# Performance work log

Measured on AMD Instinct MI355X. Metric: run time of the kernel, lower is better.

The kernel has to match this reference:

```python
import jax, jax.numpy as jnp
import numpy as np

VOXEL_SIZE = 0.1
MAX_GS_PER_VOXEL = 2
CONF_W, OPAC_W = 0.7, 0.3
CONF_THRESH, OPAC_THRESH = 0.1, 0.01
VOX_OFFSET, VOX_BITS = 512, 10  # pack 3 voxel coords into 30-bit int32 key


def _erp_directions(H, W, img_h, img_w):
    # Equirectangular ray directions, [H, W, 3]
    fx = img_w / (2.0 * np.pi)
    fy = -img_h / np.pi
    cx, cy = img_w / 2.0, img_h / 2.0
    u = jnp.arange(W, dtype=jnp.float32)
    v = jnp.arange(H, dtype=jnp.float32)
    uu, vv = jnp.meshgrid(u, v, indexing='xy')  # [H, W]
    lon = (uu + 0.5 - cx) / fx
    lat = (vv + 0.5 - cy) / fy
    cos_lat = jnp.cos(lat)
    return jnp.stack([cos_lat * jnp.sin(lon), jnp.sin(-lat), cos_lat * jnp.cos(lon)], axis=-1)


def _select_per_batch(vid, neg_score, valid_i):
    # vid: [P] int32 voxel ids (invalid -> INT32_MAX sentinel, sorts last)
    # per-voxel top-k by score via sort + segmented rank; returns bool [P] selection mask
    P = vid.shape[0]
    idx = jnp.arange(P, dtype=jnp.int32)
    vid_s, _, idx_s, valid_s = jax.lax.sort((vid, neg_score, idx, valid_i), num_keys=2)
    is_new = jnp.concatenate([jnp.ones((1,), bool), vid_s[1:] != vid_s[:-1]])
    seg_start = jax.lax.cummax(jnp.where(is_new, idx, 0), axis=0)
    rank = idx - seg_start  # rank within voxel, best score first
    sel_s = (rank < MAX_GS_PER_VOXEL) & (valid_s == 1)
    return jnp.zeros((P,), bool).at[idx_s].set(sel_s)


def _forward(depth, covariance, rotation, opacity, sh_color, confidence, poses, img_h, img_w):
    B, N, H, W = depth.shape
    P = N * H * W
    dirs = _erp_directions(H, W, img_h, img_w)  # [H,W,3]
    pts_cam = depth[..., None] * dirs  # [B,N,H,W,3]
    R = poses[:, :, :3, :3]
    t = poses[:, :, :3, 3]
    pts_world = jnp.einsum('bnij,bnhwj->bnhwi', R, pts_cam) + t[:, :, None, None, :]
    means = pts_world.reshape(B, P, 3)
    scales = covariance.transpose(0, 1, 3, 4, 2).reshape(B, P, 3)
    rots = rotation.transpose(0, 1, 3, 4, 2).reshape(B, P, 4)
    opac = opacity.reshape(B, P, 1)
    shs = sh_color.transpose(0, 1, 3, 4, 2).reshape(B, P, -1)
    conf = confidence.reshape(B, P, 1)
    valid = (conf[..., 0] > CONF_THRESH) & (opac[..., 0] > OPAC_THRESH)
    score = CONF_W * conf[..., 0] + OPAC_W * opac[..., 0]
    # voxel binning: packed 30-bit voxel id per point
    vc = jnp.clip(jnp.floor(means / VOXEL_SIZE).astype(jnp.int32) + VOX_OFFSET, 0, (1 << VOX_BITS) - 1)
    vid = (vc[..., 0] << (2 * VOX_BITS)) | (vc[..., 1] << VOX_BITS) | vc[..., 2]
    vid = jnp.where(valid, vid, jnp.int32(2**31 - 1))
    sel = jax.vmap(_select_per_batch)(vid, -score, valid.astype(jnp.int32))  # [B,P]
    feat = jnp.concatenate([means, scales, rots, opac, shs, conf], axis=-1)  # [B,P,24]
    return feat * sel[..., None].astype(feat.dtype), sel


def setup_inputs() -> dict:
    key = jax.random.key(0)
    ks = jax.random.split(key, 7)
    B, N, H, W, C = 2, 4, 256, 512, 12
    return {
        'depth': jax.random.uniform(ks[0], (B, N, H, W), jnp.float32),
        'covariance': jax.random.uniform(ks[1], (B, N, 3, H, W), jnp.float32),
        'rotation': jax.random.normal(ks[2], (B, N, 4, H, W), jnp.float32),
        'opacity': jax.random.uniform(ks[3], (B, N, H, W), jnp.float32),
        'sh_color': jax.random.normal(ks[4], (B, N, C, H, W), jnp.float32),
        'confidence': jax.random.uniform(ks[5], (B, N, H, W), jnp.float32),
        'poses': jax.random.normal(ks[6], (B, N, 4, 4), jnp.float32),
        'img_h': 256,
        'img_w': 512,
    }


def reference(depth, covariance, rotation, opacity, sh_color, confidence, poses, img_h, img_w):
    return _forward(depth, covariance, rotation, opacity, sh_color, confidence, poses, img_h, img_w)
```

## Files before the change

### kernel.cpp

```cpp
#include <hip/hip_runtime.h>
#include <stdint.h>
#include <math.h>

#ifndef M_PI
#define M_PI 3.14159265358979323846
#endif

#define B_ 2
#define N_ 4
#define H_ 256
#define W_ 512
#define C_ 12
#define HW_ (H_*W_)
#define P_ (N_*HW_)
#define BP_ (B_*P_)
#define INVALID_ENTRY 0xFFFFFFFFu

#define CHUNK 1024
#define PPT 4
#define LTAB 2048
#define LMASK (LTAB-1)
#define PROBE_MAX 8

__device__ __forceinline__ uint32_t mix32(uint32_t k) {
    k ^= k >> 16; k *= 0x85ebca6bu;
    k ^= k >> 13; k *= 0xc2b2ae35u;
    k ^= k >> 16;
    return k;
}

__device__ __forceinline__ void compute_means(
    int b, int n, float d, const float* __restrict__ tab,
    const float* __restrict__ poses, int h, int w, float m[3])
{
    float sin_lon  = tab[w];
    float cos_lon  = tab[W_ + w];
    float cos_lat  = tab[2*W_ + h];
    float sin_nlat = tab[2*W_ + H_ + h];

    float pc0 = __fmul_rn(d, __fmul_rn(cos_lat, sin_lon));
    float pc1 = __fmul_rn(d, sin_nlat);
    float pc2 = __fmul_rn(d, __fmul_rn(cos_lat, cos_lon));

    const float* Pz = poses + (size_t)(b * N_ + n) * 16;
#pragma unroll
    for (int i = 0; i < 3; ++i) {
        float s = __fmul_rn(Pz[i*4+0], pc0);
        s = __fadd_rn(s, __fmul_rn(Pz[i*4+1], pc1));
        s = __fadd_rn(s, __fmul_rn(Pz[i*4+2], pc2));
        s = __fadd_rn(s, Pz[i*4+3]);
        m[i] = s;
    }
}

__device__ __forceinline__ unsigned long long make_pk(float conf, float opac, int p) {
    float score = __fadd_rn(__fmul_rn(0.7f, conf), __fmul_rn(0.3f, opac));
    return ((unsigned long long)__float_as_uint(score) << 32)
         | (unsigned long long)(~(uint32_t)p);
}

__device__ __forceinline__ uint32_t voxel_key(const float m[3], int b) {
    int vc[3];
#pragma unroll
    for (int i = 0; i < 3; ++i) {
        float q  = __fdiv_rn(m[i], 0.1f);
        float fq = floorf(q);
        int vi = (int)fq + 512;
        vi = vi < 0 ? 0 : (vi > 1023 ? 1023 : vi);
        vc[i] = vi;
    }
    uint32_t vid = ((uint32_t)vc[0] << 20) | ((uint32_t)vc[1] << 10) | (uint32_t)vc[2];
    return vid | ((uint32_t)b << 30) | 0x80000000u;
}

__device__ __forceinline__ uint32_t gfind(uint32_t* __restrict__ keys,
                                          uint32_t key, uint32_t tmask) {
    uint32_t slot = mix32(key) & tmask;
    while (true) {
        uint32_t k = keys[slot];
        if (k == key) return slot;
        if (k == 0u) {
            uint32_t prev = atomicCAS(&keys[slot], 0u, key);
            if (prev == 0u || prev == key) return slot;
        }
        slot = (slot + 1) & tmask;
    }
}

__device__ __forceinline__ void gmerge(ulonglong2* __restrict__ slots, uint32_t slot,
                                       unsigned long long a, unsigned long long b) {
    ulonglong2 sp = slots[slot];
    unsigned long long low = a;
    if (a > sp.x) {
        unsigned long long old = atomicMax(&slots[slot].x, a);
        low = old < a ? old : a;
    }
    unsigned long long push = low > b ? low : b;
    if (push != 0ull && push > sp.y) atomicMax(&slots[slot].y, push);
}

__global__ __launch_bounds__(256) void k_dirs(
    const int* __restrict__ p_imh, const int* __restrict__ p_imw,
    float* __restrict__ tab)
{
    int i = blockIdx.x * blockDim.x + threadIdx.x;
    int imh = *p_imh, imw = *p_imw;
    float fxf = (float)((double)imw / (2.0 * M_PI));
    float fyf = (float)(-(double)imh / M_PI);
    float cxf = (float)imw * 0.5f;
    float cyf = (float)imh * 0.5f;
    if (i < W_) {
        float lon = __fdiv_rn(__fsub_rn(__fadd_rn((float)i, 0.5f), cxf), fxf);
        double dlon = (double)lon;
        tab[i]       = (float)sin(dlon);
        tab[W_ + i]  = (float)cos(dlon);
    } else if (i < W_ + H_) {
        int h = i - W_;
        float lat = __fdiv_rn(__fsub_rn(__fadd_rn((float)h, 0.5f), cyf), fyf);
        double dlat = (double)lat;
        tab[2*W_ + h]       = (float)cos(dlat);
        tab[2*W_ + H_ + h]  = (float)sin(-dlat);
    }
}

__global__ __launch_bounds__(256) void k_pass1(
    const float* __restrict__ depth,
    const float* __restrict__ opacity,
    const float* __restrict__ confidence,
    const float* __restrict__ poses,
    const float* __restrict__ tab,
    uint32_t* __restrict__ keys,
    ulonglong2* __restrict__ slots,
    uint32_t* __restrict__ entry_arr,
    uint32_t tmask)
{
    __shared__ uint32_t           lkey[LTAB];
    __shared__ unsigned long long ls0[LTAB];
    __shared__ unsigned long long ls1[LTAB];
    __shared__ uint32_t           lgs[LTAB];

    for (int i = threadIdx.x; i < LTAB; i += 256) {
        lkey[i] = 0u; ls0[i] = 0ull; ls1[i] = 0ull;
    }
    __syncthreads();

    const int base = blockIdx.x * CHUNK;

    uint32_t           mykey[PPT];
    unsigned long long mypk[PPT];
    int                myl[PPT];

#pragma unroll
    for (int k = 0; k < PPT; ++k) {
        int g  = base + threadIdx.x + k * 256;
        int b  = g >> 19;
        int p  = g & (P_ - 1);
        int n  = p >> 17;
        int hw = p & (HW_ - 1);
        int h  = hw >> 9;
        int w  = hw & (W_ - 1);

        float conf = confidence[g];
        float opac = opacity[g];
        bool valid = (conf > 0.1f) && (opac > 0.01f);
        myl[k] = -1;
        if (!valid) continue;

        float m[3];
        compute_means(b, n, depth[g], tab, poses, h, w, m);
        uint32_t key = voxel_key(m, b);
        unsigned long long pk = make_pk(conf, opac, p);
        mykey[k] = key; mypk[k] = pk;

        uint32_t sl = mix32(key) & LMASK;
        int found = -1;
#pragma unroll 1
        for (int pr = 0; pr < PROBE_MAX; ++pr) {
            uint32_t kk = atomicCAS(&lkey[sl], 0u, key);
            if (kk == 0u || kk == key) { found = (int)sl; break; }
            sl = (sl + 1) & LMASK;
        }
        if (found >= 0) {
            unsigned long long old = atomicMax(&ls0[found], pk);
            unsigned long long low = old < pk ? old : pk;
            if (low != 0ull) atomicMax(&ls1[found], low);
            myl[k] = found;
        } else {
            myl[k] = -2;
        }
    }
    __syncthreads();

    for (int i = threadIdx.x; i < LTAB; i += 256) {
        uint32_t key = lkey[i];
        if (key == 0u) continue;
        uint32_t slot = gfind(keys, key, tmask);
        lgs[i] = slot;
        gmerge(slots, slot, ls0[i], ls1[i]);
    }
    __syncthreads();

#pragma unroll
    for (int k = 0; k < PPT; ++k) {
        int g = base + threadIdx.x + k * 256;
        uint32_t e;
        if (myl[k] == -1) {
            e = INVALID_ENTRY;
        } else if (myl[k] >= 0) {
            e = lgs[myl[k]];
        } else {
            uint32_t slot = gfind(keys, mykey[k], tmask);
            gmerge(slots, slot, mypk[k], 0ull);
            e = slot;
        }
        entry_arr[g] = e;
    }
}

__global__ __launch_bounds__(256) void k_pass3(
    const float* __restrict__ depth,
    const float* __restrict__ covariance,
    const float* __restrict__ rotation,
    const float* __restrict__ opacity,
    const float* __restrict__ sh_color,
    const float* __restrict__ confidence,
    const float* __restrict__ poses,
    const float* __restrict__ tab,
    const uint32_t* __restrict__ entry_arr,
    const ulonglong2* __restrict__ slots,
    float* __restrict__ out)
{
    int g = blockIdx.x * blockDim.x + threadIdx.x;
    if (g >= BP_) return;
    int b  = g >> 19;
    int p  = g & (P_ - 1);
    int n  = p >> 17;
    int hw = p & (HW_ - 1);
    int h  = hw >> 9;
    int w  = hw & (W_ - 1);

    float conf = confidence[g];
    float opac = opacity[g];

    uint32_t e = entry_arr[g];
    bool sel = false;
    if (e != INVALID_ENTRY) {
        unsigned long long pk = make_pk(conf, opac, p);
        ulonglong2 sp = slots[e];
        sel = (pk == sp.x) || (pk == sp.y);
    }

    alignas(16) float v[24];
    if (sel) {
        float m[3];
        compute_means(b, n, depth[g], tab, poses, h, w, m);
        int bn = b * N_ + n;
        const float* cov = covariance + (size_t)bn * 3  * HW_ + hw;
        const float* rot = rotation   + (size_t)bn * 4  * HW_ + hw;
        const float* shc = sh_color   + (size_t)bn * 12 * HW_ + hw;
        v[0] = m[0]; v[1] = m[1]; v[2] = m[2];
        v[3] = cov[0]; v[4] = cov[HW_]; v[5] = cov[2*HW_];
        v[6] = rot[0]; v[7] = rot[HW_]; v[8] = rot[2*HW_]; v[9] = rot[3*HW_];
        v[10] = opac;
#pragma unroll
        for (int c = 0; c < 12; ++c) v[11 + c] = shc[(size_t)c * HW_];
        v[23] = conf;
    } else {
#pragma unroll
        for (int i = 0; i < 24; ++i) v[i] = 0.0f;
    }

    float4* o = (float4*)(out + (size_t)g * 24);
#pragma unroll
    for (int i = 0; i < 6; ++i) o[i] = ((const float4*)v)[i];

    out[(size_t)BP_ * 24 + g] = sel ? 1.0f : 0.0f;
}

extern "C" void kernel_launch(void* const* d_in, const int* in_sizes, int n_in,
                              void* d_out, int out_size, void* d_ws, size_t ws_size,
                              hipStream_t stream)
{
    const float* depth      = (const float*)d_in[0];
    const float* covariance = (const float*)d_in[1];
    const float* rotation   = (const float*)d_in[2];
    const float* opacity    = (const float*)d_in[3];
    const float* sh_color   = (const float*)d_in[4];
    const float* confidence = (const float*)d_in[5];
    const float* poses      = (const float*)d_in[6];
    const int*   imh        = (const int*)d_in[7];
    const int*   imw        = (const int*)d_in[8];
    float* out = (float*)d_out;

    size_t tab_bytes = (size_t)(2*W_ + 2*H_) * 4;
    size_t fixed_bytes = (size_t)BP_ * 4 + tab_bytes;
    size_t T = (size_t)1 << 20;
    while (T > ((size_t)1 << 18) && fixed_bytes + T * 20 > ws_size) T >>= 1;

    char* wp = (char*)d_ws;
    uint32_t* keys     = (uint32_t*)wp;   wp += T * 4;
    ulonglong2* slots  = (ulonglong2*)wp; wp += T * 16;
    uint32_t* entry_a  = (uint32_t*)wp;   wp += (size_t)BP_ * 4;
    float* tab = (float*)wp;              wp += tab_bytes;

    hipMemsetAsync(d_ws, 0x00, T * 20, stream);

    dim3 blk(256);
    hipLaunchKernelGGL(k_dirs, dim3((2*W_ + 2*H_ + 255) / 256), blk, 0, stream,
                       imh, imw, tab);

    hipLaunchKernelGGL(k_pass1, dim3(BP_ / CHUNK), blk, 0, stream,
                       depth, opacity, confidence, poses, tab,
                       keys, slots, entry_a, (uint32_t)(T - 1));
    hipLaunchKernelGGL(k_pass3, dim3(BP_ / 256), blk, 0, stream,
                       depth, covariance, rotation, opacity, sh_color, confidence,
                       poses, tab, entry_a, slots, out);
}
```

Baseline: 307.3 us.

## Stage pass3 outputs through LDS for coalesced nontemporal vector stores

Pass3 now loads every feature for all points without branching, multiplies each by the selection mask, and writes them into a transposed shared-memory tile. It then writes coalesced float4 rows to the output with nontemporal stores. Previously each thread wrote six strided float4s and loaded features only for selected points. This improves write coalescing and keeps streaming output out of cache, but reads all inputs even for unselected points and adds LDS traffic plus a barrier. Pass1 also reuses the lkey array for global slot ids, dropping the separate lgs array to cut shared memory.

```diff
diff --git a/kernel.cpp b/kernel.cpp
--- a/kernel.cpp
+++ b/kernel.cpp
@@ -22,6 +22,8 @@
 #define LMASK (LTAB-1)
 #define PROBE_MAX 8
 
+typedef float fx4 __attribute__((ext_vector_type(4)));
+
 __device__ __forceinline__ uint32_t mix32(uint32_t k) {
     k ^= k >> 16; k *= 0x85ebca6bu;
     k ^= k >> 13; k *= 0xc2b2ae35u;
@@ -29,15 +31,10 @@
     return k;
 }
 
-__device__ __forceinline__ void compute_means(
-    int b, int n, float d, const float* __restrict__ tab,
-    const float* __restrict__ poses, int h, int w, float m[3])
-{
-    float sin_lon  = tab[w];
-    float cos_lon  = tab[W_ + w];
-    float cos_lat  = tab[2*W_ + h];
-    float sin_nlat = tab[2*W_ + H_ + h];
-
+__device__ __forceinline__ void compute_means_raw(
+    int b, int n, float d, float sin_lon, float cos_lon, float cos_lat, float sin_nlat,
+    const float* __restrict__ poses, float m[3])
+{
     float pc0 = __fmul_rn(d, __fmul_rn(cos_lat, sin_lon));
     float pc1 = __fmul_rn(d, sin_nlat);
     float pc2 = __fmul_rn(d, __fmul_rn(cos_lat, cos_lon));
@@ -51,6 +48,14 @@
         s = __fadd_rn(s, Pz[i*4+3]);
         m[i] = s;
     }
+}
+
+__device__ __forceinline__ void compute_means(
+    int b, int n, float d, const float* __restrict__ tab,
+    const float* __restrict__ poses, int h, int w, float m[3])
+{
+    compute_means_raw(b, n, d, tab[w], tab[W_ + w], tab[2*W_ + h], tab[2*W_ + H_ + h],
+                      poses, m);
 }
 
 __device__ __forceinline__ unsigned long long make_pk(float conf, float opac, int p) {
@@ -137,7 +142,6 @@
     __shared__ uint32_t           lkey[LTAB];
     __shared__ unsigned long long ls0[LTAB];
     __shared__ unsigned long long ls1[LTAB];
-    __shared__ uint32_t           lgs[LTAB];
 
     for (int i = threadIdx.x; i < LTAB; i += 256) {
         lkey[i] = 0u; ls0[i] = 0ull; ls1[i] = 0ull;
@@ -195,8 +199,8 @@
         uint32_t key = lkey[i];
         if (key == 0u) continue;
         uint32_t slot = gfind(keys, key, tmask);
-        lgs[i] = slot;
         gmerge(slots, slot, ls0[i], ls1[i]);
+        lkey[i] = slot;
     }
     __syncthreads();
 
@@ -207,7 +211,7 @@
         if (myl[k] == -1) {
             e = INVALID_ENTRY;
         } else if (myl[k] >= 0) {
-            e = lgs[myl[k]];
+            e = lkey[myl[k]];
         } else {
             uint32_t slot = gfind(keys, mykey[k], tmask);
             gmerge(slots, slot, mypk[k], 0ull);
@@ -230,51 +234,67 @@
     const ulonglong2* __restrict__ slots,
     float* __restrict__ out)
 {
-    int g = blockIdx.x * blockDim.x + threadIdx.x;
-    if (g >= BP_) return;
+    __shared__ float st[25 * 256];
+
+    const int tid = threadIdx.x;
+    const int g   = blockIdx.x * 256 + tid;
     int b  = g >> 19;
     int p  = g & (P_ - 1);
     int n  = p >> 17;
     int hw = p & (HW_ - 1);
     int h  = hw >> 9;
     int w  = hw & (W_ - 1);
-
+    int bn = b * N_ + n;
+
+    float d    = depth[g];
     float conf = confidence[g];
     float opac = opacity[g];
-
     uint32_t e = entry_arr[g];
+
     bool sel = false;
     if (e != INVALID_ENTRY) {
         unsigned long long pk = make_pk(conf, opac, p);
         ulonglong2 sp = slots[e];
         sel = (pk == sp.x) || (pk == sp.y);
     }
-
-    alignas(16) float v[24];
-    if (sel) {
-        float m[3];
-        compute_means(b, n, depth[g], tab, poses, h, w, m);
-        int bn = b * N_ + n;
-        const float* cov = covariance + (size_t)bn * 3  * HW_ + hw;
-        const float* rot = rotation   + (size_t)bn * 4  * HW_ + hw;
-        const float* shc = sh_color   + (size_t)bn * 12 * HW_ + hw;
-        v[0] = m[0]; v[1] = m[1]; v[2] = m[2];
-        v[3] = cov[0]; v[4] = cov[HW_]; v[5] = cov[2*HW_];
-        v[6] = rot[0]; v[7] = rot[HW_]; v[8] = rot[2*HW_]; v[9] = rot[3*HW_];
-        v[10] = opac;
-#pragma unroll
-        for (int c = 0; c < 12; ++c) v[11 + c] = shc[(size_t)c * HW_];
-        v[23] = conf;
-    } else {
-#pragma unroll
-        for (int i = 0; i < 24; ++i) v[i] = 0.0f;
-    }
-
-    float4* o = (float4*)(out + (size_t)g * 24);
-#pragma unroll
-    for (int i = 0; i < 6; ++i) o[i] = ((const float4*)v)[i];
-
-    out[(size_t)BP_ * 24 + g] = sel ? 1.0f : 0.0f;
+    float msk = sel ? 1.0f : 0.0f;
+
+    float m[3];
+    compute_means(b, n, d, tab, poses, h, w, m);
+
+    const float* cov = covariance + (size_t)bn * 3  * HW_ + hw;
+    const float* rot = rotation   + (size_t)bn * 4  * HW_ + hw;
+    const float* shc = sh_color   + (size_t)bn * 12 * HW_ + hw;
+
+    st[0*256 + tid] = m[0] * msk;
+    st[1*256 + tid] = m[1] * msk;
+    st[2*256 + tid] = m[2] * msk;
+#pragma unroll
+    for (int c = 0; c < 3; ++c)  st[(3 + c)*256 + tid]  = cov[(size_t)c * HW_] * msk;
+#pragma unroll
+    for (int c = 0; c < 4; ++c)  st[(6 + c)*256 + tid]  = rot[(size_t)c * HW_] * msk;
+    st[10*256 + tid] = opac * msk;
+#pragma unroll
+    for (int c = 0; c < 12; ++c) st[(11 + c)*256 + tid] = shc[(size_t)c * HW_] * msk;
+    st[23*256 + tid] = conf * msk;
+    st[24*256 + tid] = msk;
+
+    __syncthreads();
+
+    fx4* obase = (fx4*)(out + (size_t)blockIdx.x * 256 * 24);
+#pragma unroll
+    for (int s = 0; s < 6; ++s) {
+        int k = s * 256 + tid;
+        int pt = k / 6;
+        int oq = k - pt * 6;
+        fx4 f;
+        f.x = st[(oq*4 + 0)*256 + pt];
+        f.y = st[(oq*4 + 1)*256 + pt];
+        f.z = st[(oq*4 + 2)*256 + pt];
+        f.w = st[(oq*4 + 3)*256 + pt];
+        __builtin_nontemporal_store(f, &obase[k]);
+    }
+    __builtin_nontemporal_store(st[24*256 + tid], &out[(size_t)BP_ * 24 + g]);
 }
 
 extern "C" void kernel_launch(void* const* d_in, const int* in_sizes, int n_in,
@@ -303,7 +323,7 @@
     uint32_t* entry_a  = (uint32_t*)wp;   wp += (size_t)BP_ * 4;
     float* tab = (float*)wp;              wp += tab_bytes;
 
-    hipMemsetAsync(d_ws, 0x00, T * 20, stream);
+    (void)hipMemsetAsync(d_ws, 0x00, T * 20, stream);
 
     dim3 blk(256);
     hipLaunchKernelGGL(k_dirs, dim3((2*W_ + 2*H_ + 255) / 256), blk, 0, stream,
```

New measurement: 262.5 us. 14.6% less time.
